# Kernel optimization log

Hardware: AMD Instinct MI355X
Metric: run time of the kernel (lower is better)

## Reference

```python
import jax, jax.numpy as jnp
import numpy as np

B, NP, NL, CIN, COUT, MID = 2048, 8, 4, 256, 256, 64


def setup_inputs() -> dict:
    key = jax.random.key(0)
    ks = jax.random.split(key, 16)
    s = 0.01  # small init scale (code uses xavier_normal with tiny gain)
    inp = {
        "x": jax.random.normal(ks[0], (B, CIN), jnp.float32),
        "h": jax.random.normal(ks[1], (B, NP), jnp.float32),
        "index": jnp.zeros((NL,), jnp.float32).at[0].set(1.0),  # one-hot layer index
        # target Linear params
        "target_w": jax.random.normal(ks[2], (COUT, CIN), jnp.float32) * (1.0 / np.sqrt(CIN)),
        "target_b": jax.random.normal(ks[3], (COUT,), jnp.float32) * 0.01,
        # embedder weight branch
        "fcwp_w": jax.random.normal(ks[4], (MID * CIN, NP), jnp.float32) * s,
        "fcwp_b": jnp.zeros((MID * CIN,), jnp.float32),
        "fcwi_w": jax.random.normal(ks[5], (MID * CIN, NL), jnp.float32) * s,
        "fcwi_b": jnp.zeros((MID * CIN,), jnp.float32),
        "fcwe_w": jax.random.normal(ks[6], (COUT, MID), jnp.float32) * s,
        "fcwe_b": jnp.zeros((COUT,), jnp.float32),
        # embedder bias branch
        "fcbp_w": jax.random.normal(ks[7], (COUT, NP), jnp.float32) * s,
        "fcbp_b": jnp.zeros((COUT,), jnp.float32),
        "fcbi_w": jax.random.normal(ks[8], (COUT, NL), jnp.float32) * s,
        "fcbi_b": jnp.zeros((COUT,), jnp.float32),
    }
    return inp


def reference(x, h, index, target_w, target_b,
              fcwp_w, fcwp_b, fcwi_w, fcwi_b, fcwe_w, fcwe_b,
              fcbp_w, fcbp_b, fcbi_w, fcbi_b):
    # --- embedder: per-sample weight modulation ---
    # w_flat: (B, mid*cin)
    w_flat = h @ fcwp_w.T + fcwp_b + (index @ fcwi_w.T + fcwi_b)
    w = w_flat.reshape(B, CIN, MID)                      # (B, cin, mid)
    w = jnp.einsum('bim,om->boi', w, fcwe_w) + fcwe_b[None, :, None]  # swapaxes folded in -> (B, out, cin)
    # bias modulation: (B, out)
    b = h @ fcbp_w.T + fcbp_b + (index @ fcbi_w.T + fcbi_b)
    # --- per-sample linear (grouped conv2d == batched GEMM) ---
    weights = target_w[None] + w                         # (B, out, cin)
    y = jnp.einsum('bi,boi->bo', x, weights)             # batched matvec
    y = y + target_b[None, :] + b
    return y
```

## Files before the change

kernel.cpp:

```cpp
#include <hip/hip_runtime.h>


#define B_TOT 2048
#define NP    8
#define CIN   256
#define COUT  256
#define MID   64
#define LDA   264
#define LDB   264
#define LDY   66
#define LDT   72
#define LDA2  104

typedef short  short8  __attribute__((ext_vector_type(8)));
typedef float  floatx4 __attribute__((ext_vector_type(4)));

__device__ __forceinline__ unsigned short f2bf(float f) {
    union { float f; unsigned u; } v; v.f = f;
    unsigned r = v.u + 0x7FFFu + ((v.u >> 16) & 1u);
    return (unsigned short)(r >> 16);
}
__device__ __forceinline__ float bf2f(unsigned short u) {
    union { unsigned u; float f; } v; v.u = ((unsigned)u) << 16;
    return v.f;
}

__global__ __launch_bounds__(256) void setup_kernel(
    const float* __restrict__ index,
    const float* __restrict__ target_w, const float* __restrict__ target_b,
    const float* __restrict__ fcwp_w, const float* __restrict__ fcwp_b,
    const float* __restrict__ fcwi_w, const float* __restrict__ fcwi_b,
    const float* __restrict__ fcwe_w, const float* __restrict__ fcwe_b,
    const float* __restrict__ fcbp_w, const float* __restrict__ fcbp_b,
    const float* __restrict__ fcbi_w, const float* __restrict__ fcbi_b,
    unsigned short* __restrict__ Bb, unsigned short* __restrict__ B2)
{
    int gid = blockIdx.x * 256 + threadIdx.x;
    if (gid < 131072) {
        int e = gid;
        int n = e & 511, i = e >> 9;
        Bb[n * CIN + i] = f2bf(fcwp_w[e]);
    } else if (gid < 147456) {
        int e = gid - 131072;
        int i = e >> 6, m = e & 63;
        float v = fcwp_b[e] + fcwi_b[e]
                + index[0] * fcwi_w[e * 4]     + index[1] * fcwi_w[e * 4 + 1]
                + index[2] * fcwi_w[e * 4 + 2] + index[3] * fcwi_w[e * 4 + 3];
        Bb[(512 + m) * CIN + i] = f2bf(v);
    } else if (gid < 212992) {
        int e = gid - 147456;
        Bb[576 * CIN + e] = f2bf(target_w[e]);
    } else if (gid < 229376) {
        int e = gid - 212992;
        int o = e >> 6, m = e & 63;
        B2[o * 96 + m] = f2bf(fcwe_w[e]);
    } else if (gid < 231424) {
        int e = gid - 229376;
        int o = e >> 3, p = e & 7;
        B2[o * 96 + 64 + p] = f2bf(fcbp_w[e]);
    } else if (gid < 231680) {
        int o = gid - 231424;
        B2[o * 96 + 72] = f2bf(fcwe_b[o]);
        float bc = target_b[o] + fcbp_b[o] + fcbi_b[o]
                 + index[0] * fcbi_w[o * 4]     + index[1] * fcbi_w[o * 4 + 1]
                 + index[2] * fcbi_w[o * 4 + 2] + index[3] * fcbi_w[o * 4 + 3];
        B2[o * 96 + 73] = f2bf(bc);
        #pragma unroll
        for (int z = 74; z < 96; ++z) B2[o * 96 + z] = 0;
    }
}

__global__ __launch_bounds__(256) void fused_kernel(
    const float* __restrict__ x,
    const float* __restrict__ h,
    const unsigned short* __restrict__ Bb,
    const unsigned short* __restrict__ B2,
    float* __restrict__ out)
{
    __shared__ unsigned short As[16 * LDA];
    __shared__ unsigned short Bs[64 * LDB];
    __shared__ float Yt[16 * LDY];
    __shared__ float tl[16][LDT];
    __shared__ float hl[16][NP];
    __shared__ float ps[16][16];
    __shared__ float sxl[16];
    __shared__ unsigned short A2[16 * LDA2];

    const int tid  = threadIdx.x;
    const int lane = tid & 63, w = tid >> 6;
    const int col  = lane & 15, quad = lane >> 4;
    const int b0   = blockIdx.x * 16;

    #pragma unroll
    for (int it = 0; it < 4; ++it) {
        int idx = it * 256 + tid;
        int r = idx >> 6, c = (idx & 63) * 4;
        float4 v = *(const float4*)(x + (size_t)(b0 + r) * CIN + c);
        ushort4 o4;
        o4.x = f2bf(v.x); o4.y = f2bf(v.y); o4.z = f2bf(v.z); o4.w = f2bf(v.w);
        *(ushort4*)&As[r * LDA + c] = o4;
    }
    if (tid < 16 * NP) hl[tid >> 3][tid & 7] = h[(size_t)b0 * NP + tid];
    __syncthreads();

    {
        int s = tid >> 4, seg = tid & 15;
        float p = 0.f;
        #pragma unroll
        for (int j = 0; j < 16; ++j) p += bf2f(As[s * LDA + seg * 16 + j]);
        ps[s][seg] = p;
    }
    __syncthreads();
    if (tid < 16) {
        float p = 0.f;
        #pragma unroll
        for (int j = 0; j < 16; ++j) p += ps[tid][j];
        sxl[tid] = p;
    }

    floatx4 ybase[4];

    for (int nt = 0; nt < 13; ++nt) {
        __syncthreads();
        #pragma unroll
        for (int it = 0; it < 8; ++it) {
            int idx = it * 256 + tid;
            int r = idx >> 5, ch = (idx & 31) * 8;
            uint4 v = *(const uint4*)(Bb + (size_t)(nt * 64 + r) * CIN + ch);
            *(uint4*)&Bs[r * LDB + ch] = v;
        }
        __syncthreads();

        floatx4 acc = floatx4{0.f, 0.f, 0.f, 0.f};
        #pragma unroll
        for (int ks = 0; ks < 8; ++ks) {
            int kc = ks * 32 + quad * 8;
            short8 af = *(const short8*)&As[col * LDA + kc];
            short8 bf = *(const short8*)&Bs[(w * 16 + col) * LDB + kc];
            acc = __builtin_amdgcn_mfma_f32_16x16x32_bf16(af, bf, acc, 0, 0, 0);
        }

        if (nt < 8) {
            #pragma unroll
            for (int r = 0; r < 4; ++r)
                Yt[(quad * 4 + r) * LDY + w * 16 + col] = acc[r];
            __syncthreads();
            if (tid < 128) {
                int s = tid >> 3, ml = tid & 7;
                float tv = 0.f;
                #pragma unroll
                for (int p = 0; p < NP; ++p)
                    tv += hl[s][p] * Yt[s * LDY + ml * 8 + p];
                tl[s][nt * 8 + ml] = tv;
            }
        } else if (nt == 8) {
            #pragma unroll
            for (int r = 0; r < 4; ++r)
                Yt[(quad * 4 + r) * LDY + w * 16 + col] = acc[r];
            __syncthreads();
            #pragma unroll
            for (int it = 0; it < 4; ++it) {
                int idx = it * 256 + tid;
                int s = idx >> 6, m = idx & 63;
                tl[s][m] += Yt[s * LDY + m];
            }
        } else {
            ybase[nt - 9] = acc;
        }
    }
    __syncthreads();

    #pragma unroll
    for (int it = 0; it < 4; ++it) {
        int idx = it * 256 + tid;
        int s = idx >> 6, m = idx & 63;
        A2[s * LDA2 + m] = f2bf(tl[s][m]);
    }
    if (tid < 128) A2[(tid >> 3) * LDA2 + 64 + (tid & 7)] = f2bf(hl[tid >> 3][tid & 7]);
    if (tid < 16) {
        A2[tid * LDA2 + 72] = f2bf(sxl[tid]);
        A2[tid * LDA2 + 73] = 0x3F80;
    }
    for (int idx = tid; idx < 16 * 22; idx += 256) {
        int s = idx / 22, cc = 74 + idx % 22;
        A2[s * LDA2 + cc] = 0;
    }
    __syncthreads();

    floatx4 y2[4];
    #pragma unroll
    for (int j = 0; j < 4; ++j) y2[j] = ybase[j];
    #pragma unroll
    for (int ks = 0; ks < 3; ++ks) {
        int kc = ks * 32 + quad * 8;
        short8 af = *(const short8*)&A2[col * LDA2 + kc];
        #pragma unroll
        for (int j = 0; j < 4; ++j) {
            short8 bf = *(const short8*)(B2 + (size_t)(j * 64 + w * 16 + col) * 96 + kc);
            y2[j] = __builtin_amdgcn_mfma_f32_16x16x32_bf16(af, bf, y2[j], 0, 0, 0);
        }
    }
    #pragma unroll
    for (int j = 0; j < 4; ++j)
        #pragma unroll
        for (int r = 0; r < 4; ++r)
            out[(size_t)(b0 + quad * 4 + r) * COUT + j * 64 + w * 16 + col] = y2[j][r];
}

extern "C" void kernel_launch(void* const* d_in, const int* in_sizes, int n_in,
                              void* d_out, int out_size, void* d_ws, size_t ws_size,
                              hipStream_t stream) {
    const float* x        = (const float*)d_in[0];
    const float* h        = (const float*)d_in[1];
    const float* index    = (const float*)d_in[2];
    const float* target_w = (const float*)d_in[3];
    const float* target_b = (const float*)d_in[4];
    const float* fcwp_w   = (const float*)d_in[5];
    const float* fcwp_b   = (const float*)d_in[6];
    const float* fcwi_w   = (const float*)d_in[7];
    const float* fcwi_b   = (const float*)d_in[8];
    const float* fcwe_w   = (const float*)d_in[9];
    const float* fcwe_b   = (const float*)d_in[10];
    const float* fcbp_w   = (const float*)d_in[11];
    const float* fcbp_b   = (const float*)d_in[12];
    const float* fcbi_w   = (const float*)d_in[13];
    const float* fcbi_b   = (const float*)d_in[14];
    float* out = (float*)d_out;

    char* ws = (char*)d_ws;
    unsigned short* Bb = (unsigned short*)ws;
    unsigned short* B2 = (unsigned short*)(ws + 425984);

    setup_kernel<<<905, 256, 0, stream>>>(
        index, target_w, target_b, fcwp_w, fcwp_b, fcwi_w, fcwi_b,
        fcwe_w, fcwe_b, fcbp_w, fcbp_b, fcbi_w, fcbi_b, Bb, B2);

    fused_kernel<<<B_TOT / 16, 256, 0, stream>>>(x, h, Bb, B2, out);
}
```

Before: 99.90 us.

## Double-buffer weight tiles with register prefetch and shuffle-reduce the h contraction

The fused kernel now double-buffers the B tile in shared memory and prefetches the next 64-row tile into registers while the current one is computed. This removes one barrier per iteration and hides global load latency. The h-weighted reduction uses wave shuffles in place of a shared Yt staging buffer, and the MFMA chain is split into two independent accumulators. The setup kernel is rewritten to use vectorized loads and an LDS-tiled transpose, which cuts it from 905 to 69 blocks and adds register pressure from the 8 uint4 prefetch registers.

```diff
diff --git a/kernel.cpp b/kernel.cpp
--- a/kernel.cpp
+++ b/kernel.cpp
@@ -8,7 +8,6 @@
 #define MID   64
 #define LDA   264
 #define LDB   264
-#define LDY   66
 #define LDT   72
 #define LDA2  104
 
@@ -35,31 +34,83 @@
     const float* __restrict__ fcbi_w, const float* __restrict__ fcbi_b,
     unsigned short* __restrict__ Bb, unsigned short* __restrict__ B2)
 {
-    int gid = blockIdx.x * 256 + threadIdx.x;
-    if (gid < 131072) {
-        int e = gid;
-        int n = e & 511, i = e >> 9;
-        Bb[n * CIN + i] = f2bf(fcwp_w[e]);
-    } else if (gid < 147456) {
-        int e = gid - 131072;
-        int i = e >> 6, m = e & 63;
-        float v = fcwp_b[e] + fcwi_b[e]
-                + index[0] * fcwi_w[e * 4]     + index[1] * fcwi_w[e * 4 + 1]
-                + index[2] * fcwi_w[e * 4 + 2] + index[3] * fcwi_w[e * 4 + 3];
-        Bb[(512 + m) * CIN + i] = f2bf(v);
-    } else if (gid < 212992) {
-        int e = gid - 147456;
-        Bb[576 * CIN + e] = f2bf(target_w[e]);
-    } else if (gid < 229376) {
-        int e = gid - 212992;
+    __shared__ unsigned short Lt[64][68];
+    const int blk = blockIdx.x, tid = threadIdx.x;
+
+    if (blk < 32) {
+        const int i0 = (blk >> 3) * 64, n0 = (blk & 7) * 64;
+        const int r = tid >> 4, c4 = (tid & 15) * 4;
+        #pragma unroll
+        for (int k = 0; k < 4; ++k) {
+            int ii = r + k * 16;
+            float4 v = *(const float4*)(fcwp_w + (size_t)(i0 + ii) * 512 + n0 + c4);
+            Lt[c4 + 0][ii] = f2bf(v.x); Lt[c4 + 1][ii] = f2bf(v.y);
+            Lt[c4 + 2][ii] = f2bf(v.z); Lt[c4 + 3][ii] = f2bf(v.w);
+        }
+        __syncthreads();
+        const int nn = tid >> 2, ic0 = (tid & 3) * 16;
+        #pragma unroll
+        for (int k = 0; k < 4; ++k) {
+            int ic = ic0 + k * 4;
+            ushort4 o4;
+            o4.x = Lt[nn][ic]; o4.y = Lt[nn][ic + 1];
+            o4.z = Lt[nn][ic + 2]; o4.w = Lt[nn][ic + 3];
+            *(ushort4*)&Bb[(size_t)(n0 + nn) * CIN + i0 + ic] = o4;
+        }
+    } else if (blk < 36) {
+        const int i0 = (blk - 32) * 64;
+        const float x0 = index[0], x1 = index[1], x2 = index[2], x3 = index[3];
+        const int r = tid >> 4, c4 = (tid & 15) * 4;
+        #pragma unroll
+        for (int k = 0; k < 4; ++k) {
+            int ii = r + k * 16;
+            int e = (i0 + ii) * 64 + c4;
+            float4 pb = *(const float4*)(fcwp_b + e);
+            float4 ib = *(const float4*)(fcwi_b + e);
+            float pbv[4] = {pb.x, pb.y, pb.z, pb.w};
+            float ibv[4] = {ib.x, ib.y, ib.z, ib.w};
+            #pragma unroll
+            for (int j = 0; j < 4; ++j) {
+                float4 wv = *(const float4*)(fcwi_w + (size_t)(e + j) * 4);
+                float val = pbv[j] + ibv[j]
+                          + x0 * wv.x + x1 * wv.y + x2 * wv.z + x3 * wv.w;
+                Lt[c4 + j][ii] = f2bf(val);
+            }
+        }
+        __syncthreads();
+        const int mm = tid >> 2, ic0 = (tid & 3) * 16;
+        #pragma unroll
+        for (int k = 0; k < 4; ++k) {
+            int ic = ic0 + k * 4;
+            ushort4 o4;
+            o4.x = Lt[mm][ic]; o4.y = Lt[mm][ic + 1];
+            o4.z = Lt[mm][ic + 2]; o4.w = Lt[mm][ic + 3];
+            *(ushort4*)&Bb[(size_t)(512 + mm) * CIN + i0 + ic] = o4;
+        }
+    } else if (blk < 52) {
+        #pragma unroll
+        for (int k = 0; k < 4; ++k) {
+            int e = (blk - 36) * 4096 + k * 1024 + tid * 4;
+            float4 v = *(const float4*)(target_w + e);
+            ushort4 o4;
+            o4.x = f2bf(v.x); o4.y = f2bf(v.y); o4.z = f2bf(v.z); o4.w = f2bf(v.w);
+            *(ushort4*)&Bb[(size_t)576 * CIN + e] = o4;
+        }
+    } else if (blk < 68) {
+        int e = (blk - 52) * 1024 + tid * 4;
         int o = e >> 6, m = e & 63;
-        B2[o * 96 + m] = f2bf(fcwe_w[e]);
-    } else if (gid < 231424) {
-        int e = gid - 229376;
-        int o = e >> 3, p = e & 7;
-        B2[o * 96 + 64 + p] = f2bf(fcbp_w[e]);
-    } else if (gid < 231680) {
-        int o = gid - 231424;
+        float4 v = *(const float4*)(fcwe_w + e);
+        ushort4 o4;
+        o4.x = f2bf(v.x); o4.y = f2bf(v.y); o4.z = f2bf(v.z); o4.w = f2bf(v.w);
+        *(ushort4*)&B2[(size_t)o * 96 + m] = o4;
+    } else {
+        int o = tid;
+        float4 p0 = *(const float4*)(fcbp_w + (size_t)o * 8);
+        float4 p1 = *(const float4*)(fcbp_w + (size_t)o * 8 + 4);
+        B2[o * 96 + 64] = f2bf(p0.x); B2[o * 96 + 65] = f2bf(p0.y);
+        B2[o * 96 + 66] = f2bf(p0.z); B2[o * 96 + 67] = f2bf(p0.w);
+        B2[o * 96 + 68] = f2bf(p1.x); B2[o * 96 + 69] = f2bf(p1.y);
+        B2[o * 96 + 70] = f2bf(p1.z); B2[o * 96 + 71] = f2bf(p1.w);
         B2[o * 96 + 72] = f2bf(fcwe_b[o]);
         float bc = target_b[o] + fcbp_b[o] + fcbi_b[o]
                  + index[0] * fcbi_w[o * 4]     + index[1] * fcbi_w[o * 4 + 1]
@@ -78,8 +129,7 @@
     float* __restrict__ out)
 {
     __shared__ unsigned short As[16 * LDA];
-    __shared__ unsigned short Bs[64 * LDB];
-    __shared__ float Yt[16 * LDY];
+    __shared__ unsigned short Bs[2][64 * LDB];
     __shared__ float tl[16][LDT];
     __shared__ float hl[16][NP];
     __shared__ float ps[16][16];
@@ -103,6 +153,10 @@
     if (tid < 16 * NP) hl[tid >> 3][tid & 7] = h[(size_t)b0 * NP + tid];
     __syncthreads();
 
+    float hr[4];
+    #pragma unroll
+    for (int r = 0; r < 4; ++r) hr[r] = hl[quad * 4 + r][col & 7];
+
     {
         int s = tid >> 4, seg = tid & 15;
         float p = 0.f;
@@ -118,54 +172,71 @@
         sxl[tid] = p;
     }
 
+    uint4 pf[8];
+    #pragma unroll
+    for (int it = 0; it < 8; ++it) {
+        int idx = it * 256 + tid;
+        pf[it] = *(const uint4*)(Bb + (size_t)(idx >> 5) * CIN + (idx & 31) * 8);
+    }
+
     floatx4 ybase[4];
 
     for (int nt = 0; nt < 13; ++nt) {
-        __syncthreads();
+        unsigned short* bs = Bs[nt & 1];
         #pragma unroll
         for (int it = 0; it < 8; ++it) {
             int idx = it * 256 + tid;
-            int r = idx >> 5, ch = (idx & 31) * 8;
-            uint4 v = *(const uint4*)(Bb + (size_t)(nt * 64 + r) * CIN + ch);
-            *(uint4*)&Bs[r * LDB + ch] = v;
+            *(uint4*)&bs[(idx >> 5) * LDB + (idx & 31) * 8] = pf[it];
+        }
+        if (nt < 12) {
+            const unsigned short* src = Bb + (size_t)(nt + 1) * 64 * CIN;
+            #pragma unroll
+            for (int it = 0; it < 8; ++it) {
+                int idx = it * 256 + tid;
+                pf[it] = *(const uint4*)(src + (size_t)(idx >> 5) * CIN + (idx & 31) * 8);
+            }
         }
         __syncthreads();
 
-        floatx4 acc = floatx4{0.f, 0.f, 0.f, 0.f};
-        #pragma unroll
-        for (int ks = 0; ks < 8; ++ks) {
-            int kc = ks * 32 + quad * 8;
-            short8 af = *(const short8*)&As[col * LDA + kc];
-            short8 bf = *(const short8*)&Bs[(w * 16 + col) * LDB + kc];
-            acc = __builtin_amdgcn_mfma_f32_16x16x32_bf16(af, bf, acc, 0, 0, 0);
+        floatx4 a0 = floatx4{0.f, 0.f, 0.f, 0.f};
+        floatx4 a1 = floatx4{0.f, 0.f, 0.f, 0.f};
+        #pragma unroll
+        for (int ks = 0; ks < 4; ++ks) {
+            int kc0 = ks * 32 + quad * 8;
+            int kc1 = 128 + kc0;
+            short8 af0 = *(const short8*)&As[col * LDA + kc0];
+            short8 bf0 = *(const short8*)&bs[(w * 16 + col) * LDB + kc0];
+            a0 = __builtin_amdgcn_mfma_f32_16x16x32_bf16(af0, bf0, a0, 0, 0, 0);
+            short8 af1 = *(const short8*)&As[col * LDA + kc1];
+            short8 bf1 = *(const short8*)&bs[(w * 16 + col) * LDB + kc1];
+            a1 = __builtin_amdgcn_mfma_f32_16x16x32_bf16(af1, bf1, a1, 0, 0, 0);
         }
 
         if (nt < 8) {
-            #pragma unroll
-            for (int r = 0; r < 4; ++r)
-                Yt[(quad * 4 + r) * LDY + w * 16 + col] = acc[r];
-            __syncthreads();
-            if (tid < 128) {
-                int s = tid >> 3, ml = tid & 7;
-                float tv = 0.f;
+            float u[4];
+            #pragma unroll
+            for (int r = 0; r < 4; ++r) u[r] = (a0[r] + a1[r]) * hr[r];
+            #pragma unroll
+            for (int r = 0; r < 4; ++r) {
+                u[r] += __shfl_xor(u[r], 1);
+                u[r] += __shfl_xor(u[r], 2);
+                u[r] += __shfl_xor(u[r], 4);
+            }
+            if ((col & 7) == 0) {
+                int m = nt * 8 + 2 * w + (col >> 3);
                 #pragma unroll
-                for (int p = 0; p < NP; ++p)
-                    tv += hl[s][p] * Yt[s * LDY + ml * 8 + p];
-                tl[s][nt * 8 + ml] = tv;
+                for (int r = 0; r < 4; ++r) tl[quad * 4 + r][m] = u[r];
             }
         } else if (nt == 8) {
+            __syncthreads();
             #pragma unroll
             for (int r = 0; r < 4; ++r)
-                Yt[(quad * 4 + r) * LDY + w * 16 + col] = acc[r];
-            __syncthreads();
-            #pragma unroll
-            for (int it = 0; it < 4; ++it) {
-                int idx = it * 256 + tid;
-                int s = idx >> 6, m = idx & 63;
-                tl[s][m] += Yt[s * LDY + m];
-            }
+                tl[quad * 4 + r][w * 16 + col] += a0[r] + a1[r];
         } else {
-            ybase[nt - 9] = acc;
+            floatx4 s;
+            #pragma unroll
+            for (int r = 0; r < 4; ++r) s[r] = a0[r] + a1[r];
+            ybase[nt - 9] = s;
         }
     }
     __syncthreads();
@@ -231,7 +302,7 @@
     unsigned short* Bb = (unsigned short*)ws;
     unsigned short* B2 = (unsigned short*)(ws + 425984);
 
-    setup_kernel<<<905, 256, 0, stream>>>(
+    setup_kernel<<<69, 256, 0, stream>>>(
         index, target_w, target_b, fcwp_w, fcwp_b, fcwi_w, fcwi_b,
         fcwe_w, fcwe_b, fcbp_w, fcbp_b, fcbi_w, fcbi_b, Bb, B2);
 
```

After: 127.3 us. 1.27x slower.
